# Kernel optimization log

Hardware: AMD Instinct MI355X
Metric: run time of the kernel (lower is better)

Reference implementation:

```python
import jax, jax.numpy as jnp
import numpy as np

C_IN = 256
K = 4
C_QK = C_IN // K  # 64


def setup_inputs() -> dict:
    key = jax.random.key(0)
    ks = jax.random.split(key, 9)
    B, C, H, W = 4, C_IN, 64, 64
    s = 0.02
    return {
        "x": jax.random.normal(ks[0], (B, C, H, W), dtype=jnp.float32),
        # 1x1 convs stored as dense [out, in] matrices (kernel_size=1)
        "wq": jax.random.normal(ks[1], (C_QK, C), dtype=jnp.float32) * s,
        "bq": jax.random.normal(ks[2], (C_QK,), dtype=jnp.float32) * s,
        "wk": jax.random.normal(ks[3], (C_QK, C), dtype=jnp.float32) * s,
        "bk": jax.random.normal(ks[4], (C_QK,), dtype=jnp.float32) * s,
        "wv": jax.random.normal(ks[5], (C, C), dtype=jnp.float32) * s,
        "bv": jax.random.normal(ks[6], (C,), dtype=jnp.float32) * s,
        "wg": jax.random.normal(ks[7], (C, C), dtype=jnp.float32) * s,
        "bg": jax.random.normal(ks[8], (C,), dtype=jnp.float32) * s,
    }


def reference(x, wq, bq, wk, bk, wv, bv, wg, bg):
    B, C, H, W = x.shape
    N = H * W
    xf = x.reshape(B, C, N)  # [B, C, N]
    # 1x1 conv == per-pixel linear over channels
    q = jnp.einsum("oc,bcn->bon", wq, xf) + bq[None, :, None]  # [B, Cqk, N]
    k = jnp.einsum("oc,bcn->bon", wk, xf) + bk[None, :, None]  # [B, Cqk, N]
    v = jnp.einsum("oc,bcn->bon", wv, xf) + bv[None, :, None]  # [B, C, N]
    # energy[b, n, m] = <q[:, n], k[:, m]>  (n = query pos, m = key pos)
    energy = jnp.einsum("bon,bom->bnm", q, k)  # [B, N, N]
    energy = jax.nn.elu(energy) / N
    # out[b, c, m] = sum_n v[b, c, n] * energy[b, n, m]
    out = jnp.einsum("bcn,bnm->bcm", v, energy).reshape(B, C, H, W)
    out = jnp.einsum("oc,bchw->bohw", wg, out) + bg[None, :, None, None]
    return out
```

## Files before the change

kernel.cpp:

```cpp
#include <hip/hip_runtime.h>

#define B_ 4
#define C_ 256
#define CQK 64
#define N_ 4096
#define SEG 2
#define SEGN (N_ / SEG)
#define NB 128
#define ITERS (SEGN / NB)
#define TS 512

typedef _Float16 f16;
typedef __attribute__((ext_vector_type(8))) _Float16 f16x8;
typedef __attribute__((ext_vector_type(4))) _Float16 f16x4;
typedef __attribute__((ext_vector_type(4))) float f32x4;
typedef __attribute__((ext_vector_type(4))) float float4v;

#define TILE_OFF(l15, quad) ((l15) * 32 + (quad) * 8)

__global__ __launch_bounds__(256) void prep_w(
    const float* __restrict__ wq, const float* __restrict__ wk,
    const float* __restrict__ wv, const float* __restrict__ wg,
    f16* __restrict__ WQt, f16* __restrict__ WKt, f16* __restrict__ WVt,
    f16* __restrict__ WGt) {
  int chunk = blockIdx.x * 256 + threadIdx.x;
  if (chunk >= 20480) return;
  const float* src;
  f16* dst;
  int lo;
  if (chunk < 2048) { src = wq; dst = WQt; lo = chunk * 8; }
  else if (chunk < 4096) { src = wk; dst = WKt; lo = (chunk - 2048) * 8; }
  else if (chunk < 12288) { src = wv; dst = WVt; lo = (chunk - 4096) * 8; }
  else { src = wg; dst = WGt; lo = (chunk - 12288) * 8; }
  int o = lo >> 8, k = lo & 255;
  f16x8 v;
#pragma unroll
  for (int j = 0; j < 8; j++) v[j] = (f16)src[lo + j];
  *(f16x8*)(dst + ((size_t)(o >> 4) * 8 + (k >> 5)) * TS + (o & 15) * 32 + (k & 31)) = v;
}

__global__ __launch_bounds__(512) void proj(
    const float* __restrict__ x, const f16* __restrict__ WQt,
    const f16* __restrict__ WKt, const f16* __restrict__ WVt,
    const float* __restrict__ bq, const float* __restrict__ bk,
    const float* __restrict__ bv, f16* __restrict__ QTt, f16* __restrict__ KTt,
    f16* __restrict__ Vt) {
  __shared__ float xs[64][65];
  __shared__ f16 xt[4 * 8 * TS];
  int n0 = blockIdx.x * 64;
  int b = blockIdx.y;
  int tid = threadIdx.x, lane = tid & 63, w = tid >> 6;
  int l15 = lane & 15, quad = lane >> 4;
  const float* xb = x + (size_t)b * C_ * N_;

  for (int cc = 0; cc < 4; cc++) {
#pragma unroll
    for (int i = 0; i < 8; i++)
      xs[lane][w * 8 + i] = xb[(size_t)(cc * 64 + w * 8 + i) * N_ + n0 + lane];
    __syncthreads();
    {
      int nt = w >> 1;
      f16x8 v;
#pragma unroll
      for (int j = 0; j < 8; j++)
        v[j] = (f16)xs[nt * 16 + l15][32 * (w & 1) + quad * 8 + j];
      *(f16x8*)(xt + (nt * 8 + cc * 2 + (w & 1)) * TS + l15 * 32 + quad * 8) = v;
    }
    __syncthreads();
  }

  f32x4 acc[3][4];
#pragma unroll
  for (int j = 0; j < 3; j++)
#pragma unroll
    for (int nt = 0; nt < 4; nt++) acc[j][nt] = (f32x4){0.f, 0.f, 0.f, 0.f};

#pragma unroll
  for (int kt = 0; kt < 8; kt++) {
    f16x8 xf[4];
#pragma unroll
    for (int nt = 0; nt < 4; nt++)
      xf[nt] = *(const f16x8*)(xt + (nt * 8 + kt) * TS + TILE_OFF(l15, quad));
#pragma unroll
    for (int j = 0; j < 3; j++) {
      int g = w * 3 + j;
      const f16* Wt;
      int ot;
      bool isV = g < 16;
      if (isV) { Wt = WVt; ot = g; }
      else if (g < 20) { Wt = WQt; ot = g - 16; }
      else { Wt = WKt; ot = g - 20; }
      f16x8 wf = *(const f16x8*)(Wt + ((size_t)ot * 8 + kt) * TS + TILE_OFF(l15, quad));
#pragma unroll
      for (int nt = 0; nt < 4; nt++)
        acc[j][nt] = isV
            ? __builtin_amdgcn_mfma_f32_16x16x32_f16(xf[nt], wf, acc[j][nt], 0, 0, 0)
            : __builtin_amdgcn_mfma_f32_16x16x32_f16(wf, xf[nt], acc[j][nt], 0, 0, 0);
    }
  }

  f16* vbout = Vt + (size_t)b * C_ * N_;
#pragma unroll
  for (int j = 0; j < 3; j++) {
    int g = w * 3 + j;
    if (g < 16) {
      float bvv = bv[16 * g + l15];
#pragma unroll
      for (int nt = 0; nt < 4; nt++) {
        f16x4 vals;
#pragma unroll
        for (int r = 0; r < 4; r++) vals[r] = (f16)(acc[j][nt][r] + bvv);
        *(f16x4*)(vbout + ((size_t)g * 128 + (n0 >> 5) + (nt >> 1)) * TS +
                  l15 * 32 + 16 * (nt & 1) + 4 * quad) = vals;
      }
    } else {
      int oq = (g < 20) ? (g - 16) : (g - 20);
      const float* bias = (g < 20) ? bq : bk;
      f16* ob = ((g < 20) ? QTt : KTt) + (size_t)b * N_ * CQK;
#pragma unroll
      for (int nt = 0; nt < 4; nt++) {
        f16x4 vals;
#pragma unroll
        for (int r = 0; r < 4; r++)
          vals[r] = (f16)(acc[j][nt][r] + bias[16 * oq + 4 * quad + r]);
        *(f16x4*)(ob + (((size_t)(n0 >> 4) + nt) * 2 + (oq >> 1)) * TS + l15 * 32 +
                  16 * (oq & 1) + 4 * quad) = vals;
      }
    }
  }
}

__global__ __launch_bounds__(256, 2) void attn(const f16* __restrict__ qt,
                                               const f16* __restrict__ kt,
                                               const f16* __restrict__ v,
                                               const f16* __restrict__ WGt,
                                               float* __restrict__ part) {
  __shared__ __align__(16) f16 sPt[2][64][128];
  int m0 = blockIdx.x * 64;
  int seg = blockIdx.y;
  int b = blockIdx.z;
  int tid = threadIdx.x, lane = tid & 63, w = tid >> 6;
  int l15 = lane & 15, quad = lane >> 4;
  const f16* qtb = qt + (size_t)b * N_ * CQK;
  const f16* ktb = kt + (size_t)b * N_ * CQK;
  const f16* vb = v + (size_t)b * C_ * N_;

  f32x4 oacc[4][4];
#pragma unroll
  for (int ct = 0; ct < 4; ct++)
#pragma unroll
    for (int mt = 0; mt < 4; mt++) oacc[ct][mt] = (f32x4){0.f, 0.f, 0.f, 0.f};

  f16x8 kf[4][2];
#pragma unroll
  for (int mt = 0; mt < 4; mt++)
#pragma unroll
    for (int ks = 0; ks < 2; ks++)
      kf[mt][ks] = *(const f16x8*)(ktb + ((size_t)((m0 >> 4) + mt) * 2 + ks) * TS +
                                   TILE_OFF(l15, quad));

  f16x8 qf[2][2];
  {
    int nq = seg * SEGN;
#pragma unroll
    for (int nt = 0; nt < 2; nt++)
#pragma unroll
      for (int ks = 0; ks < 2; ks++)
        qf[nt][ks] = *(const f16x8*)(qtb +
                                     ((size_t)((nq >> 4) + 2 * w + nt) * 2 + ks) * TS +
                                     TILE_OFF(l15, quad));
  }

  for (int it = 0; it < ITERS; it++) {
    int n0 = seg * SEGN + it * NB;
    f16x8 vfA[2][4];
#pragma unroll
    for (int ks = 0; ks < 2; ks++)
#pragma unroll
      for (int ct = 0; ct < 4; ct++)
        vfA[ks][ct] = *(const f16x8*)(vb +
                                      ((size_t)(4 * w + ct) * 128 + (n0 >> 5) + ks) * TS +
                                      TILE_OFF(l15, quad));

    char* buf = (char*)sPt[it & 1];
#pragma unroll
    for (int nt = 0; nt < 2; nt++) {
      f32x4 sacc[4];
#pragma unroll
      for (int mt = 0; mt < 4; mt++) sacc[mt] = (f32x4){0.f, 0.f, 0.f, 0.f};
#pragma unroll
      for (int ks = 0; ks < 2; ks++)
#pragma unroll
        for (int mt = 0; mt < 4; mt++)
          sacc[mt] = __builtin_amdgcn_mfma_f32_16x16x32_f16(qf[nt][ks], kf[mt][ks],
                                                            sacc[mt], 0, 0, 0);
#pragma unroll
      for (int mt = 0; mt < 4; mt++) {
        f16x4 p;
#pragma unroll
        for (int r = 0; r < 4; r++) {
          float s = sacc[mt][r];
          p[r] = (f16)(s > 0.0f ? s : (__expf(s) - 1.0f));
        }
        int row = 16 * mt + l15;
        int colb = (64 * w + 32 * nt + 8 * quad) ^ ((row & 7) << 4);
        *(f16x4*)(buf + row * 256 + colb) = p;
      }
    }
    __syncthreads();

    f16x8 vfB[2][4];
    f16x8 pa[4];
#pragma unroll
    for (int mt = 0; mt < 4; mt++) {
      int row = 16 * mt + l15;
      pa[mt] = *(const f16x8*)(buf + row * 256 + ((quad * 16) ^ ((row & 7) << 4)));
    }
#pragma unroll
    for (int ks = 0; ks < 2; ks++)
#pragma unroll
      for (int ct = 0; ct < 4; ct++)
        vfB[ks][ct] = *(const f16x8*)(vb + ((size_t)(4 * w + ct) * 128 + (n0 >> 5) +
                                            2 + ks) * TS +
                                      TILE_OFF(l15, quad));
#pragma unroll
    for (int ct = 0; ct < 4; ct++)
#pragma unroll
      for (int mt = 0; mt < 4; mt++)
        oacc[ct][mt] = __builtin_amdgcn_mfma_f32_16x16x32_f16(vfA[0][ct], pa[mt],
                                                              oacc[ct][mt], 0, 0, 0);
    if (it + 1 < ITERS) {
      int nq = n0 + NB;
#pragma unroll
      for (int nt = 0; nt < 2; nt++)
#pragma unroll
        for (int ks = 0; ks < 2; ks++)
          qf[nt][ks] = *(const f16x8*)(qtb +
                                       ((size_t)((nq >> 4) + 2 * w + nt) * 2 + ks) * TS +
                                       TILE_OFF(l15, quad));
    }
#pragma unroll
    for (int mt = 0; mt < 4; mt++) {
      int row = 16 * mt + l15;
      pa[mt] = *(const f16x8*)(buf + row * 256 + ((64 + quad * 16) ^ ((row & 7) << 4)));
    }
#pragma unroll
    for (int ct = 0; ct < 4; ct++)
#pragma unroll
      for (int mt = 0; mt < 4; mt++)
        oacc[ct][mt] = __builtin_amdgcn_mfma_f32_16x16x32_f16(vfA[1][ct], pa[mt],
                                                              oacc[ct][mt], 0, 0, 0);
#pragma unroll
    for (int mt = 0; mt < 4; mt++) {
      int row = 16 * mt + l15;
      pa[mt] = *(const f16x8*)(buf + row * 256 + ((128 + quad * 16) ^ ((row & 7) << 4)));
    }
#pragma unroll
    for (int ct = 0; ct < 4; ct++)
#pragma unroll
      for (int mt = 0; mt < 4; mt++)
        oacc[ct][mt] = __builtin_amdgcn_mfma_f32_16x16x32_f16(vfB[0][ct], pa[mt],
                                                              oacc[ct][mt], 0, 0, 0);
#pragma unroll
    for (int mt = 0; mt < 4; mt++) {
      int row = 16 * mt + l15;
      pa[mt] = *(const f16x8*)(buf + row * 256 + ((192 + quad * 16) ^ ((row & 7) << 4)));
    }
#pragma unroll
    for (int ct = 0; ct < 4; ct++)
#pragma unroll
      for (int mt = 0; mt < 4; mt++)
        oacc[ct][mt] = __builtin_amdgcn_mfma_f32_16x16x32_f16(vfB[1][ct], pa[mt],
                                                              oacc[ct][mt], 0, 0, 0);
  }

  __syncthreads();
  f16* obuf = (f16*)sPt;
#pragma unroll
  for (int ct = 0; ct < 4; ct++) {
#pragma unroll
    for (int mt = 0; mt < 4; mt++) {
      f16x4 vals;
#pragma unroll
      for (int r = 0; r < 4; r++)
        vals[r] = (f16)(oacc[ct][mt][r] * (1.0f / (float)N_));
      *(f16x4*)(obuf + (mt * 8 + 2 * w + (ct >> 1)) * TS + l15 * 32 +
                16 * (ct & 1) + 4 * quad) = vals;
    }
  }
  __syncthreads();
  f32x4 accO[4][4];
#pragma unroll
  for (int ot = 0; ot < 4; ot++)
#pragma unroll
    for (int mt = 0; mt < 4; mt++) accO[ot][mt] = (f32x4){0.f, 0.f, 0.f, 0.f};
#pragma unroll
  for (int kt = 0; kt < 8; kt++) {
    f16x8 bO[4];
#pragma unroll
    for (int mt = 0; mt < 4; mt++)
      bO[mt] = *(const f16x8*)(obuf + (mt * 8 + kt) * TS + TILE_OFF(l15, quad));
#pragma unroll
    for (int ot = 0; ot < 4; ot++) {
      f16x8 af = *(const f16x8*)(WGt + ((size_t)(4 * w + ot) * 8 + kt) * TS +
                                 TILE_OFF(l15, quad));
#pragma unroll
      for (int mt = 0; mt < 4; mt++)
        accO[ot][mt] = __builtin_amdgcn_mfma_f32_16x16x32_f16(af, bO[mt], accO[ot][mt], 0, 0, 0);
    }
  }
  float* pb = part + ((size_t)(seg * B_ + b) * C_) * N_;
#pragma unroll
  for (int ot = 0; ot < 4; ot++) {
#pragma unroll
    for (int mt = 0; mt < 4; mt++) {
      int m = m0 + 16 * mt + l15;
#pragma unroll
      for (int r = 0; r < 4; r++) {
        int o = 64 * w + 16 * ot + 4 * quad + r;
        pb[(size_t)o * N_ + m] = accO[ot][mt][r];
      }
    }
  }
}

__global__ __launch_bounds__(256) void combine(const float* __restrict__ part,
                                               const float* __restrict__ bg,
                                               float* __restrict__ out) {
  size_t i = ((size_t)blockIdx.x * 256 + threadIdx.x) * 4;
  float4v p0 = *(const float4v*)(part + i);
  float4v p1 = *(const float4v*)(part + (size_t)B_ * C_ * N_ + i);
  float bgo = bg[(i >> 12) & 255];
  float4v r = p0 + p1;
  r[0] += bgo; r[1] += bgo; r[2] += bgo; r[3] += bgo;
  *(float4v*)(out + i) = r;
}

extern "C" void kernel_launch(void* const* d_in, const int* in_sizes, int n_in,
                              void* d_out, int out_size, void* d_ws, size_t ws_size,
                              hipStream_t stream) {
  const float* x = (const float*)d_in[0];
  const float* wq = (const float*)d_in[1];
  const float* bq = (const float*)d_in[2];
  const float* wk = (const float*)d_in[3];
  const float* bk = (const float*)d_in[4];
  const float* wv = (const float*)d_in[5];
  const float* bv = (const float*)d_in[6];
  const float* wg = (const float*)d_in[7];
  const float* bg = (const float*)d_in[8];
  float* out = (float*)d_out;

  char* ws = (char*)d_ws;
  f16* QTt = (f16*)ws; ws += (size_t)B_ * N_ * CQK * sizeof(f16);
  f16* KTt = (f16*)ws; ws += (size_t)B_ * N_ * CQK * sizeof(f16);
  f16* Vt  = (f16*)ws; ws += (size_t)B_ * C_ * N_ * sizeof(f16);
  f16* WQt = (f16*)ws; ws += (size_t)CQK * C_ * sizeof(f16);
  f16* WKt = (f16*)ws; ws += (size_t)CQK * C_ * sizeof(f16);
  f16* WVt = (f16*)ws; ws += (size_t)C_ * C_ * sizeof(f16);
  f16* WGt = (f16*)ws; ws += (size_t)C_ * C_ * sizeof(f16);
  float* PART = (float*)ws; ws += (size_t)SEG * B_ * C_ * N_ * sizeof(float);

  prep_w<<<dim3(80), 256, 0, stream>>>(wq, wk, wv, wg, WQt, WKt, WVt, WGt);
  proj<<<dim3(N_ / 64, B_), 512, 0, stream>>>(x, WQt, WKt, WVt, bq, bk, bv,
                                              QTt, KTt, Vt);
  attn<<<dim3(N_ / 64, SEG, B_), 256, 0, stream>>>(QTt, KTt, Vt, WGt, PART);
  combine<<<dim3(4096), 256, 0, stream>>>(PART, bg, out);
}
```

Baseline: 161.2 us.

## Split attention block work across eight waves with halved per-wave tiles

The attention kernel moves from 256 to 512 threads per block. The eight waves split both the score tile (query rows and key columns) and the output tile (channel groups and column halves), so each wave holds half as many accumulators and fragments. V fragment loads are staggered between MFMA phases so fewer registers are live at once. The aim is higher occupancy and better latency hiding. The cost is that each wave reloads K and V fragments redundantly and more waves contend at the barriers.

```diff
diff --git a/kernel.cpp b/kernel.cpp
--- a/kernel.cpp
+++ b/kernel.cpp
@@ -130,7 +130,7 @@
   }
 }
 
-__global__ __launch_bounds__(256, 2) void attn(const f16* __restrict__ qt,
+__global__ __launch_bounds__(512, 4) void attn(const f16* __restrict__ qt,
                                                const f16* __restrict__ kt,
                                                const f16* __restrict__ v,
                                                const f16* __restrict__ WGt,
@@ -141,137 +141,144 @@
   int b = blockIdx.z;
   int tid = threadIdx.x, lane = tid & 63, w = tid >> 6;
   int l15 = lane & 15, quad = lane >> 4;
+  int nw = w & 3, mw = w >> 2;
+  int cw = w >> 1, mo = w & 1;
   const f16* qtb = qt + (size_t)b * N_ * CQK;
   const f16* ktb = kt + (size_t)b * N_ * CQK;
   const f16* vb = v + (size_t)b * C_ * N_;
 
-  f32x4 oacc[4][4];
+  f32x4 oacc[4][2];
 #pragma unroll
   for (int ct = 0; ct < 4; ct++)
 #pragma unroll
-    for (int mt = 0; mt < 4; mt++) oacc[ct][mt] = (f32x4){0.f, 0.f, 0.f, 0.f};
-
-  f16x8 kf[4][2];
-#pragma unroll
-  for (int mt = 0; mt < 4; mt++)
+    for (int mt2 = 0; mt2 < 2; mt2++) oacc[ct][mt2] = (f32x4){0.f, 0.f, 0.f, 0.f};
+
+  f16x8 kf[2][2];
+#pragma unroll
+  for (int mt2 = 0; mt2 < 2; mt2++)
 #pragma unroll
     for (int ks = 0; ks < 2; ks++)
-      kf[mt][ks] = *(const f16x8*)(ktb + ((size_t)((m0 >> 4) + mt) * 2 + ks) * TS +
-                                   TILE_OFF(l15, quad));
+      kf[mt2][ks] = *(const f16x8*)(ktb +
+                                    ((size_t)((m0 >> 4) + 2 * mw + mt2) * 2 + ks) * TS +
+                                    TILE_OFF(l15, quad));
 
   f16x8 qf[2][2];
   {
     int nq = seg * SEGN;
 #pragma unroll
-    for (int nt = 0; nt < 2; nt++)
+    for (int nt2 = 0; nt2 < 2; nt2++)
 #pragma unroll
       for (int ks = 0; ks < 2; ks++)
-        qf[nt][ks] = *(const f16x8*)(qtb +
-                                     ((size_t)((nq >> 4) + 2 * w + nt) * 2 + ks) * TS +
-                                     TILE_OFF(l15, quad));
+        qf[nt2][ks] = *(const f16x8*)(qtb +
+                                      ((size_t)((nq >> 4) + 2 * nw + nt2) * 2 + ks) * TS +
+                                      TILE_OFF(l15, quad));
   }
 
   for (int it = 0; it < ITERS; it++) {
     int n0 = seg * SEGN + it * NB;
-    f16x8 vfA[2][4];
-#pragma unroll
-    for (int ks = 0; ks < 2; ks++)
-#pragma unroll
-      for (int ct = 0; ct < 4; ct++)
-        vfA[ks][ct] = *(const f16x8*)(vb +
-                                      ((size_t)(4 * w + ct) * 128 + (n0 >> 5) + ks) * TS +
-                                      TILE_OFF(l15, quad));
+    int nc = n0 >> 5;
+    f16x8 vf0[4], vf1[4];
+#pragma unroll
+    for (int ct = 0; ct < 4; ct++)
+      vf0[ct] = *(const f16x8*)(vb + ((size_t)(4 * cw + ct) * 128 + nc) * TS +
+                                TILE_OFF(l15, quad));
 
     char* buf = (char*)sPt[it & 1];
 #pragma unroll
-    for (int nt = 0; nt < 2; nt++) {
-      f32x4 sacc[4];
-#pragma unroll
-      for (int mt = 0; mt < 4; mt++) sacc[mt] = (f32x4){0.f, 0.f, 0.f, 0.f};
+    for (int nt2 = 0; nt2 < 2; nt2++) {
+      f32x4 sacc[2];
+#pragma unroll
+      for (int mt2 = 0; mt2 < 2; mt2++) sacc[mt2] = (f32x4){0.f, 0.f, 0.f, 0.f};
 #pragma unroll
       for (int ks = 0; ks < 2; ks++)
 #pragma unroll
-        for (int mt = 0; mt < 4; mt++)
-          sacc[mt] = __builtin_amdgcn_mfma_f32_16x16x32_f16(qf[nt][ks], kf[mt][ks],
-                                                            sacc[mt], 0, 0, 0);
-#pragma unroll
-      for (int mt = 0; mt < 4; mt++) {
+        for (int mt2 = 0; mt2 < 2; mt2++)
+          sacc[mt2] = __builtin_amdgcn_mfma_f32_16x16x32_f16(qf[nt2][ks], kf[mt2][ks],
+                                                             sacc[mt2], 0, 0, 0);
+#pragma unroll
+      for (int mt2 = 0; mt2 < 2; mt2++) {
         f16x4 p;
 #pragma unroll
         for (int r = 0; r < 4; r++) {
-          float s = sacc[mt][r];
+          float s = sacc[mt2][r];
           p[r] = (f16)(s > 0.0f ? s : (__expf(s) - 1.0f));
         }
-        int row = 16 * mt + l15;
-        int colb = (64 * w + 32 * nt + 8 * quad) ^ ((row & 7) << 4);
+        int row = 16 * (2 * mw + mt2) + l15;
+        int colb = (64 * nw + 32 * nt2 + 8 * quad) ^ ((row & 7) << 4);
         *(f16x4*)(buf + row * 256 + colb) = p;
       }
     }
+#pragma unroll
+    for (int ct = 0; ct < 4; ct++)
+      vf1[ct] = *(const f16x8*)(vb + ((size_t)(4 * cw + ct) * 128 + nc + 1) * TS +
+                                TILE_OFF(l15, quad));
     __syncthreads();
 
-    f16x8 vfB[2][4];
-    f16x8 pa[4];
-#pragma unroll
-    for (int mt = 0; mt < 4; mt++) {
-      int row = 16 * mt + l15;
-      pa[mt] = *(const f16x8*)(buf + row * 256 + ((quad * 16) ^ ((row & 7) << 4)));
-    }
-#pragma unroll
-    for (int ks = 0; ks < 2; ks++)
-#pragma unroll
-      for (int ct = 0; ct < 4; ct++)
-        vfB[ks][ct] = *(const f16x8*)(vb + ((size_t)(4 * w + ct) * 128 + (n0 >> 5) +
-                                            2 + ks) * TS +
-                                      TILE_OFF(l15, quad));
-#pragma unroll
-    for (int ct = 0; ct < 4; ct++)
-#pragma unroll
-      for (int mt = 0; mt < 4; mt++)
-        oacc[ct][mt] = __builtin_amdgcn_mfma_f32_16x16x32_f16(vfA[0][ct], pa[mt],
-                                                              oacc[ct][mt], 0, 0, 0);
+    f16x8 pa[2];
+#pragma unroll
+    for (int mt2 = 0; mt2 < 2; mt2++) {
+      int row = 16 * (2 * mo + mt2) + l15;
+      pa[mt2] = *(const f16x8*)(buf + row * 256 + ((quad * 16) ^ ((row & 7) << 4)));
+    }
+#pragma unroll
+    for (int ct = 0; ct < 4; ct++)
+#pragma unroll
+      for (int mt2 = 0; mt2 < 2; mt2++)
+        oacc[ct][mt2] = __builtin_amdgcn_mfma_f32_16x16x32_f16(vf0[ct], pa[mt2],
+                                                               oacc[ct][mt2], 0, 0, 0);
+    f16x8 vf2[4];
+#pragma unroll
+    for (int ct = 0; ct < 4; ct++)
+      vf2[ct] = *(const f16x8*)(vb + ((size_t)(4 * cw + ct) * 128 + nc + 2) * TS +
+                                TILE_OFF(l15, quad));
     if (it + 1 < ITERS) {
       int nq = n0 + NB;
 #pragma unroll
-      for (int nt = 0; nt < 2; nt++)
+      for (int nt2 = 0; nt2 < 2; nt2++)
 #pragma unroll
         for (int ks = 0; ks < 2; ks++)
-          qf[nt][ks] = *(const f16x8*)(qtb +
-                                       ((size_t)((nq >> 4) + 2 * w + nt) * 2 + ks) * TS +
-                                       TILE_OFF(l15, quad));
-    }
-#pragma unroll
-    for (int mt = 0; mt < 4; mt++) {
-      int row = 16 * mt + l15;
-      pa[mt] = *(const f16x8*)(buf + row * 256 + ((64 + quad * 16) ^ ((row & 7) << 4)));
-    }
-#pragma unroll
-    for (int ct = 0; ct < 4; ct++)
-#pragma unroll
-      for (int mt = 0; mt < 4; mt++)
-        oacc[ct][mt] = __builtin_amdgcn_mfma_f32_16x16x32_f16(vfA[1][ct], pa[mt],
-                                                              oacc[ct][mt], 0, 0, 0);
-#pragma unroll
-    for (int mt = 0; mt < 4; mt++) {
-      int row = 16 * mt + l15;
-      pa[mt] = *(const f16x8*)(buf + row * 256 + ((128 + quad * 16) ^ ((row & 7) << 4)));
-    }
-#pragma unroll
-    for (int ct = 0; ct < 4; ct++)
-#pragma unroll
-      for (int mt = 0; mt < 4; mt++)
-        oacc[ct][mt] = __builtin_amdgcn_mfma_f32_16x16x32_f16(vfB[0][ct], pa[mt],
-                                                              oacc[ct][mt], 0, 0, 0);
-#pragma unroll
-    for (int mt = 0; mt < 4; mt++) {
-      int row = 16 * mt + l15;
-      pa[mt] = *(const f16x8*)(buf + row * 256 + ((192 + quad * 16) ^ ((row & 7) << 4)));
-    }
-#pragma unroll
-    for (int ct = 0; ct < 4; ct++)
-#pragma unroll
-      for (int mt = 0; mt < 4; mt++)
-        oacc[ct][mt] = __builtin_amdgcn_mfma_f32_16x16x32_f16(vfB[1][ct], pa[mt],
-                                                              oacc[ct][mt], 0, 0, 0);
+          qf[nt2][ks] = *(const f16x8*)(qtb +
+                                        ((size_t)((nq >> 4) + 2 * nw + nt2) * 2 + ks) * TS +
+                                        TILE_OFF(l15, quad));
+    }
+#pragma unroll
+    for (int mt2 = 0; mt2 < 2; mt2++) {
+      int row = 16 * (2 * mo + mt2) + l15;
+      pa[mt2] = *(const f16x8*)(buf + row * 256 + ((64 + quad * 16) ^ ((row & 7) << 4)));
+    }
+#pragma unroll
+    for (int ct = 0; ct < 4; ct++)
+#pragma unroll
+      for (int mt2 = 0; mt2 < 2; mt2++)
+        oacc[ct][mt2] = __builtin_amdgcn_mfma_f32_16x16x32_f16(vf1[ct], pa[mt2],
+                                                               oacc[ct][mt2], 0, 0, 0);
+    f16x8 vf3[4];
+#pragma unroll
+    for (int ct = 0; ct < 4; ct++)
+      vf3[ct] = *(const f16x8*)(vb + ((size_t)(4 * cw + ct) * 128 + nc + 3) * TS +
+                                TILE_OFF(l15, quad));
+#pragma unroll
+    for (int mt2 = 0; mt2 < 2; mt2++) {
+      int row = 16 * (2 * mo + mt2) + l15;
+      pa[mt2] = *(const f16x8*)(buf + row * 256 + ((128 + quad * 16) ^ ((row & 7) << 4)));
+    }
+#pragma unroll
+    for (int ct = 0; ct < 4; ct++)
+#pragma unroll
+      for (int mt2 = 0; mt2 < 2; mt2++)
+        oacc[ct][mt2] = __builtin_amdgcn_mfma_f32_16x16x32_f16(vf2[ct], pa[mt2],
+                                                               oacc[ct][mt2], 0, 0, 0);
+#pragma unroll
+    for (int mt2 = 0; mt2 < 2; mt2++) {
+      int row = 16 * (2 * mo + mt2) + l15;
+      pa[mt2] = *(const f16x8*)(buf + row * 256 + ((192 + quad * 16) ^ ((row & 7) << 4)));
+    }
+#pragma unroll
+    for (int ct = 0; ct < 4; ct++)
+#pragma unroll
+      for (int mt2 = 0; mt2 < 2; mt2++)
+        oacc[ct][mt2] = __builtin_amdgcn_mfma_f32_16x16x32_f16(vf3[ct], pa[mt2],
+                                                               oacc[ct][mt2], 0, 0, 0);
   }
 
   __syncthreads();
@@ -279,46 +286,48 @@
 #pragma unroll
   for (int ct = 0; ct < 4; ct++) {
 #pragma unroll
-    for (int mt = 0; mt < 4; mt++) {
+    for (int mt2 = 0; mt2 < 2; mt2++) {
       f16x4 vals;
 #pragma unroll
       for (int r = 0; r < 4; r++)
-        vals[r] = (f16)(oacc[ct][mt][r] * (1.0f / (float)N_));
-      *(f16x4*)(obuf + (mt * 8 + 2 * w + (ct >> 1)) * TS + l15 * 32 +
-                16 * (ct & 1) + 4 * quad) = vals;
+        vals[r] = (f16)(oacc[ct][mt2][r] * (1.0f / (float)N_));
+      *(f16x4*)(obuf + ((size_t)(2 * mo + mt2) * 8 + 2 * cw + (ct >> 1)) * TS +
+                l15 * 32 + 16 * (ct & 1) + 4 * quad) = vals;
     }
   }
   __syncthreads();
-  f32x4 accO[4][4];
+  f32x4 accO[4][2];
 #pragma unroll
   for (int ot = 0; ot < 4; ot++)
 #pragma unroll
-    for (int mt = 0; mt < 4; mt++) accO[ot][mt] = (f32x4){0.f, 0.f, 0.f, 0.f};
+    for (int mt2 = 0; mt2 < 2; mt2++) accO[ot][mt2] = (f32x4){0.f, 0.f, 0.f, 0.f};
 #pragma unroll
   for (int kt = 0; kt < 8; kt++) {
-    f16x8 bO[4];
-#pragma unroll
-    for (int mt = 0; mt < 4; mt++)
-      bO[mt] = *(const f16x8*)(obuf + (mt * 8 + kt) * TS + TILE_OFF(l15, quad));
+    f16x8 bO[2];
+#pragma unroll
+    for (int mt2 = 0; mt2 < 2; mt2++)
+      bO[mt2] = *(const f16x8*)(obuf + ((size_t)(2 * mo + mt2) * 8 + kt) * TS +
+                                TILE_OFF(l15, quad));
 #pragma unroll
     for (int ot = 0; ot < 4; ot++) {
-      f16x8 af = *(const f16x8*)(WGt + ((size_t)(4 * w + ot) * 8 + kt) * TS +
+      f16x8 af = *(const f16x8*)(WGt + ((size_t)(4 * cw + ot) * 8 + kt) * TS +
                                  TILE_OFF(l15, quad));
 #pragma unroll
-      for (int mt = 0; mt < 4; mt++)
-        accO[ot][mt] = __builtin_amdgcn_mfma_f32_16x16x32_f16(af, bO[mt], accO[ot][mt], 0, 0, 0);
+      for (int mt2 = 0; mt2 < 2; mt2++)
+        accO[ot][mt2] = __builtin_amdgcn_mfma_f32_16x16x32_f16(af, bO[mt2],
+                                                               accO[ot][mt2], 0, 0, 0);
     }
   }
   float* pb = part + ((size_t)(seg * B_ + b) * C_) * N_;
 #pragma unroll
   for (int ot = 0; ot < 4; ot++) {
 #pragma unroll
-    for (int mt = 0; mt < 4; mt++) {
-      int m = m0 + 16 * mt + l15;
+    for (int mt2 = 0; mt2 < 2; mt2++) {
+      int m = m0 + 16 * (2 * mo + mt2) + l15;
 #pragma unroll
       for (int r = 0; r < 4; r++) {
-        int o = 64 * w + 16 * ot + 4 * quad + r;
-        pb[(size_t)o * N_ + m] = accO[ot][mt][r];
+        int o = 64 * cw + 16 * ot + 4 * quad + r;
+        pb[(size_t)o * N_ + m] = accO[ot][mt2][r];
       }
     }
   }
@@ -363,6 +372,6 @@
   prep_w<<<dim3(80), 256, 0, stream>>>(wq, wk, wv, wg, WQt, WKt, WVt, WGt);
   proj<<<dim3(N_ / 64, B_), 512, 0, stream>>>(x, WQt, WKt, WVt, bq, bk, bv,
                                               QTt, KTt, Vt);
-  attn<<<dim3(N_ / 64, SEG, B_), 256, 0, stream>>>(QTt, KTt, Vt, WGt, PART);
+  attn<<<dim3(N_ / 64, SEG, B_), 512, 0, stream>>>(QTt, KTt, Vt, WGt, PART);
   combine<<<dim3(4096), 256, 0, stream>>>(PART, bg, out);
 }
```

After: 189.0 us. 1.17x slower.

## Store split-K partials in fp16 and retile projection to 32-pixel blocks

Applied to the files above, without the earlier changes.

The attention kernel now writes its two per-segment partial outputs as fp16 instead of fp32, which halves the write and read traffic through the combine kernel, and combine processes 8 elements per thread. The projection kernel is retiled to 32 pixels per block with 256 threads, loading x with float4 reads into a transposed shared tile, doubling the grid size. The fp16 partials lose precision before the final sum, which may increase error against the fp32 reference.

```diff
diff --git a/kernel.cpp b/kernel.cpp
--- a/kernel.cpp
+++ b/kernel.cpp
@@ -39,51 +39,65 @@
   *(f16x8*)(dst + ((size_t)(o >> 4) * 8 + (k >> 5)) * TS + (o & 15) * 32 + (k & 31)) = v;
 }
 
-__global__ __launch_bounds__(512) void proj(
+__global__ __launch_bounds__(256) void proj(
     const float* __restrict__ x, const f16* __restrict__ WQt,
     const f16* __restrict__ WKt, const f16* __restrict__ WVt,
     const float* __restrict__ bq, const float* __restrict__ bk,
     const float* __restrict__ bv, f16* __restrict__ QTt, f16* __restrict__ KTt,
     f16* __restrict__ Vt) {
-  __shared__ float xs[64][65];
-  __shared__ f16 xt[4 * 8 * TS];
-  int n0 = blockIdx.x * 64;
+  __shared__ float xs[32][257];
+  __shared__ f16 xt[2][8][16 * 36];
+  int nx = blockIdx.x;
+  int n0 = nx * 32;
   int b = blockIdx.y;
   int tid = threadIdx.x, lane = tid & 63, w = tid >> 6;
   int l15 = lane & 15, quad = lane >> 4;
   const float* xb = x + (size_t)b * C_ * N_;
 
-  for (int cc = 0; cc < 4; cc++) {
-#pragma unroll
-    for (int i = 0; i < 8; i++)
-      xs[lane][w * 8 + i] = xb[(size_t)(cc * 64 + w * 8 + i) * N_ + n0 + lane];
-    __syncthreads();
-    {
-      int nt = w >> 1;
+  {
+    int a = tid & 7;
+    int crow = tid >> 3;
+#pragma unroll
+    for (int p = 0; p < 8; p++) {
+      int c = p * 32 + crow;
+      float4v vv = *(const float4v*)(xb + (size_t)c * N_ + n0 + a * 4);
+      int nn = a * 4;
+      xs[nn][c] = vv[0];
+      xs[nn + 1][c] = vv[1];
+      xs[nn + 2][c] = vv[2];
+      xs[nn + 3][c] = vv[3];
+    }
+  }
+  __syncthreads();
+#pragma unroll
+  for (int nt = 0; nt < 2; nt++) {
+#pragma unroll
+    for (int kk = 0; kk < 2; kk++) {
+      int kt = 2 * w + kk;
       f16x8 v;
 #pragma unroll
       for (int j = 0; j < 8; j++)
-        v[j] = (f16)xs[nt * 16 + l15][32 * (w & 1) + quad * 8 + j];
-      *(f16x8*)(xt + (nt * 8 + cc * 2 + (w & 1)) * TS + l15 * 32 + quad * 8) = v;
-    }
-    __syncthreads();
-  }
-
-  f32x4 acc[3][4];
-#pragma unroll
-  for (int j = 0; j < 3; j++)
-#pragma unroll
-    for (int nt = 0; nt < 4; nt++) acc[j][nt] = (f32x4){0.f, 0.f, 0.f, 0.f};
+        v[j] = (f16)xs[16 * nt + l15][kt * 32 + quad * 8 + j];
+      *(f16x8*)(&xt[nt][kt][l15 * 36 + quad * 8]) = v;
+    }
+  }
+  __syncthreads();
+
+  f32x4 acc[6][2];
+#pragma unroll
+  for (int j = 0; j < 6; j++)
+#pragma unroll
+    for (int nt = 0; nt < 2; nt++) acc[j][nt] = (f32x4){0.f, 0.f, 0.f, 0.f};
 
 #pragma unroll
   for (int kt = 0; kt < 8; kt++) {
-    f16x8 xf[4];
-#pragma unroll
-    for (int nt = 0; nt < 4; nt++)
-      xf[nt] = *(const f16x8*)(xt + (nt * 8 + kt) * TS + TILE_OFF(l15, quad));
-#pragma unroll
-    for (int j = 0; j < 3; j++) {
-      int g = w * 3 + j;
+    f16x8 xf[2];
+#pragma unroll
+    for (int nt = 0; nt < 2; nt++)
+      xf[nt] = *(const f16x8*)(&xt[nt][kt][l15 * 36 + quad * 8]);
+#pragma unroll
+    for (int j = 0; j < 6; j++) {
+      int g = w * 6 + j;
       const f16* Wt;
       int ot;
       bool isV = g < 16;
@@ -92,7 +106,7 @@
       else { Wt = WKt; ot = g - 20; }
       f16x8 wf = *(const f16x8*)(Wt + ((size_t)ot * 8 + kt) * TS + TILE_OFF(l15, quad));
 #pragma unroll
-      for (int nt = 0; nt < 4; nt++)
+      for (int nt = 0; nt < 2; nt++)
         acc[j][nt] = isV
             ? __builtin_amdgcn_mfma_f32_16x16x32_f16(xf[nt], wf, acc[j][nt], 0, 0, 0)
             : __builtin_amdgcn_mfma_f32_16x16x32_f16(wf, xf[nt], acc[j][nt], 0, 0, 0);
@@ -101,29 +115,29 @@
 
   f16* vbout = Vt + (size_t)b * C_ * N_;
 #pragma unroll
-  for (int j = 0; j < 3; j++) {
-    int g = w * 3 + j;
+  for (int j = 0; j < 6; j++) {
+    int g = w * 6 + j;
     if (g < 16) {
       float bvv = bv[16 * g + l15];
 #pragma unroll
-      for (int nt = 0; nt < 4; nt++) {
+      for (int nt = 0; nt < 2; nt++) {
         f16x4 vals;
 #pragma unroll
         for (int r = 0; r < 4; r++) vals[r] = (f16)(acc[j][nt][r] + bvv);
-        *(f16x4*)(vbout + ((size_t)g * 128 + (n0 >> 5) + (nt >> 1)) * TS +
-                  l15 * 32 + 16 * (nt & 1) + 4 * quad) = vals;
+        *(f16x4*)(vbout + ((size_t)g * 128 + nx) * TS + l15 * 32 + 16 * nt +
+                  4 * quad) = vals;
       }
     } else {
       int oq = (g < 20) ? (g - 16) : (g - 20);
       const float* bias = (g < 20) ? bq : bk;
       f16* ob = ((g < 20) ? QTt : KTt) + (size_t)b * N_ * CQK;
 #pragma unroll
-      for (int nt = 0; nt < 4; nt++) {
+      for (int nt = 0; nt < 2; nt++) {
         f16x4 vals;
 #pragma unroll
         for (int r = 0; r < 4; r++)
           vals[r] = (f16)(acc[j][nt][r] + bias[16 * oq + 4 * quad + r]);
-        *(f16x4*)(ob + (((size_t)(n0 >> 4) + nt) * 2 + (oq >> 1)) * TS + l15 * 32 +
+        *(f16x4*)(ob + ((size_t)(2 * nx + nt) * 2 + (oq >> 1)) * TS + l15 * 32 +
                   16 * (oq & 1) + 4 * quad) = vals;
       }
     }
@@ -134,7 +148,7 @@
                                                const f16* __restrict__ kt,
                                                const f16* __restrict__ v,
                                                const f16* __restrict__ WGt,
-                                               float* __restrict__ part) {
+                                               f16* __restrict__ part) {
   __shared__ __align__(16) f16 sPt[2][64][128];
   int m0 = blockIdx.x * 64;
   int seg = blockIdx.y;
@@ -309,7 +323,7 @@
         accO[ot][mt] = __builtin_amdgcn_mfma_f32_16x16x32_f16(af, bO[mt], accO[ot][mt], 0, 0, 0);
     }
   }
-  float* pb = part + ((size_t)(seg * B_ + b) * C_) * N_;
+  f16* pb = part + ((size_t)(seg * B_ + b) * C_) * N_;
 #pragma unroll
   for (int ot = 0; ot < 4; ot++) {
 #pragma unroll
@@ -318,22 +332,26 @@
 #pragma unroll
       for (int r = 0; r < 4; r++) {
         int o = 64 * w + 16 * ot + 4 * quad + r;
-        pb[(size_t)o * N_ + m] = accO[ot][mt][r];
+        pb[(size_t)o * N_ + m] = (f16)accO[ot][mt][r];
       }
     }
   }
 }
 
-__global__ __launch_bounds__(256) void combine(const float* __restrict__ part,
+__global__ __launch_bounds__(256) void combine(const f16* __restrict__ part,
                                                const float* __restrict__ bg,
                                                float* __restrict__ out) {
-  size_t i = ((size_t)blockIdx.x * 256 + threadIdx.x) * 4;
-  float4v p0 = *(const float4v*)(part + i);
-  float4v p1 = *(const float4v*)(part + (size_t)B_ * C_ * N_ + i);
+  size_t i = ((size_t)blockIdx.x * 256 + threadIdx.x) * 8;
+  f16x8 p0 = *(const f16x8*)(part + i);
+  f16x8 p1 = *(const f16x8*)(part + (size_t)B_ * C_ * N_ + i);
   float bgo = bg[(i >> 12) & 255];
-  float4v r = p0 + p1;
-  r[0] += bgo; r[1] += bgo; r[2] += bgo; r[3] += bgo;
-  *(float4v*)(out + i) = r;
+  float4v r0, r1;
+#pragma unroll
+  for (int j = 0; j < 4; j++) r0[j] = (float)p0[j] + (float)p1[j] + bgo;
+#pragma unroll
+  for (int j = 0; j < 4; j++) r1[j] = (float)p0[4 + j] + (float)p1[4 + j] + bgo;
+  *(float4v*)(out + i) = r0;
+  *(float4v*)(out + i + 4) = r1;
 }
 
 extern "C" void kernel_launch(void* const* d_in, const int* in_sizes, int n_in,
@@ -358,11 +376,11 @@
   f16* WKt = (f16*)ws; ws += (size_t)CQK * C_ * sizeof(f16);
   f16* WVt = (f16*)ws; ws += (size_t)C_ * C_ * sizeof(f16);
   f16* WGt = (f16*)ws; ws += (size_t)C_ * C_ * sizeof(f16);
-  float* PART = (float*)ws; ws += (size_t)SEG * B_ * C_ * N_ * sizeof(float);
+  f16* PART = (f16*)ws; ws += (size_t)SEG * B_ * C_ * N_ * sizeof(f16);
 
   prep_w<<<dim3(80), 256, 0, stream>>>(wq, wk, wv, wg, WQt, WKt, WVt, WGt);
-  proj<<<dim3(N_ / 64, B_), 512, 0, stream>>>(x, WQt, WKt, WVt, bq, bk, bv,
+  proj<<<dim3(N_ / 32, B_), 256, 0, stream>>>(x, WQt, WKt, WVt, bq, bk, bv,
                                               QTt, KTt, Vt);
   attn<<<dim3(N_ / 64, SEG, B_), 256, 0, stream>>>(QTt, KTt, Vt, WGt, PART);
-  combine<<<dim3(4096), 256, 0, stream>>>(PART, bg, out);
-}
+  combine<<<dim3(2048), 256, 0, stream>>>(PART, bg, out);
+}
```

Result: slower. 164.5 us (+2.1%).
